# Kernel tuning notes

Measured on AMD Instinct MI355X. Metric: run time of the kernel, lower is better.

The kernel has to match this reference:

```python
import jax, jax.numpy as jnp
import numpy as np

# norse LIFParameters defaults
DT = 1e-3
TAU_SYN_INV = 200.0   # 1/5e-3
TAU_MEM_INV = 100.0   # 1/1e-2
V_TH = 1.0            # v_leak = v_reset = 0
ALPHA = 100.0         # SuperSpike surrogate slope
SEQ_LEN = 10
F_MAX = 1000.0

@jax.custom_vjp
def superspike(x):
    # forward: heaviside(x > 0); backward: SuperSpike surrogate
    return (x > 0).astype(x.dtype)

def _ss_fwd(x):
    return (x > 0).astype(x.dtype), x

def _ss_bwd(x, g):
    return (g / (ALPHA * jnp.abs(x) + 1.0) ** 2,)

superspike.defvjp(_ss_fwd, _ss_bwd)

def lif_step(x, z, v, i, w_in, w_rec):
    # norse lif_step: decay, threshold, reset, then integrate synaptic current
    v_dec = v + DT * TAU_MEM_INV * (-v + i)      # v_leak = 0
    i_dec = i - DT * TAU_SYN_INV * i
    z_new = superspike(v_dec - V_TH)
    v_new = (1.0 - z_new) * v_dec                # v_reset = 0
    i_new = i_dec + x @ w_in.T + z @ w_rec.T     # uses OLD z for recurrence
    return z_new, v_new, i_new

def setup_inputs() -> dict:
    key = jax.random.key(0)
    k1, k2, k3, k4, k5 = jax.random.split(key, 5)
    B = 1048576
    return {
        "input_tensor": jax.random.uniform(k1, (B, 12), dtype=jnp.float32),
        "w_in0": jax.random.normal(k2, (6, 12), jnp.float32) * np.float32(np.sqrt(2.0 / 12)),
        "w_rec0": jax.random.normal(k3, (6, 6), jnp.float32) * np.float32(np.sqrt(2.0 / 6)),
        "w_in1": jax.random.normal(k4, (1, 6), jnp.float32) * np.float32(np.sqrt(2.0 / 6)),
        "w_rec1": jax.random.normal(k5, (1, 1), jnp.float32) * np.float32(np.sqrt(2.0)),
    }

def reference(input_tensor, w_in0, w_rec0, w_in1, w_rec1):
    B = input_tensor.shape[0]
    dtype = input_tensor.dtype
    # PoissonEncoder: spike = (rand < dt * f_max * x), shape [T, B, 12]
    u = jax.random.uniform(jax.random.key(42), (SEQ_LEN,) + input_tensor.shape, dtype=dtype)
    spike_ts = (u < DT * F_MAX * input_tensor).astype(dtype)

    def step(carry, x_t):
        z0, v0, i0, z1, v1, i1 = carry
        z0n, v0n, i0n = lif_step(x_t, z0, v0, i0, w_in0, w_rec0)
        z1n, v1n, i1n = lif_step(z0n, z1, v1, i1, w_in1, w_rec1)
        return (z0n, v0n, i0n, z1n, v1n, i1n), None

    zeros = lambda n: jnp.zeros((B, n), dtype)
    init = (zeros(6), zeros(6), zeros(6), zeros(1), zeros(1), zeros(1))
    (z0, v0, i0, z1, v1, i1), _ = jax.lax.scan(step, init, spike_ts)
    return z1  # final-timestep output spikes, [B, 1]
```

## Files before the change

### kernel.cpp

```cpp
#include <hip/hip_runtime.h>
#include <cstdint>


#define TFR(r) { x0 += x1; x1 = __builtin_amdgcn_alignbit(x1, x1, 32 - (r)); x1 ^= x0; }

__device__ __forceinline__ uint32_t tf_hash(uint32_t c) {
  uint32_t x0 = 0u;
  uint32_t x1 = c + 42u;
  TFR(13) TFR(15) TFR(26) TFR(6)
  x0 += 42u;          x1 += 0x1BD11BF1u;
  TFR(17) TFR(29) TFR(16) TFR(24)
  x0 += 0x1BD11BF0u;  x1 += 2u;
  TFR(13) TFR(15) TFR(26) TFR(6)
         x1 += 45u;
  TFR(17) TFR(29) TFR(16) TFR(24)
  x0 += 42u;          x1 += 0x1BD11BF4u;
  TFR(13) TFR(15) TFR(26) TFR(6)
  x0 += 0x1BD11BF0u;  x1 += 5u;
  return x0 ^ x1;
}

__global__ __launch_bounds__(256) void build_tables(
    const float* __restrict__ w_in0, const float* __restrict__ w_rec0,
    const float* __restrict__ w_in1, float* __restrict__ ws)
{
  int m = blockIdx.x * 256 + threadIdx.x;
  float* tin = ws;
  float* trc = ws + 32768;
  float* tw1 = ws + 33280;
  #pragma unroll
  for (int n = 0; n < 6; ++n) {
    float acc = 0.0f;
    #pragma unroll
    for (int j = 0; j < 12; ++j)
      acc = __fmaf_rn(((m >> j) & 1) ? 1.0f : 0.0f, w_in0[n * 12 + j], acc);
    tin[(m << 3) + n] = acc;
  }
  if (m < 64) {
    #pragma unroll
    for (int n = 0; n < 6; ++n) {
      float acc = 0.0f;
      #pragma unroll
      for (int j = 0; j < 6; ++j)
        acc = __fmaf_rn(((m >> j) & 1) ? 1.0f : 0.0f, w_rec0[n * 6 + j], acc);
      trc[(m << 3) + n] = acc;
    }
    float acc = 0.0f;
    #pragma unroll
    for (int j = 0; j < 6; ++j)
      acc = __fmaf_rn(((m >> j) & 1) ? 1.0f : 0.0f, w_in1[j], acc);
    tw1[m] = acc;
  }
}

__global__ __launch_bounds__(256) void snn_kernel_tbl(
    const float* __restrict__ x_in, const float* __restrict__ w_rec1,
    const float* __restrict__ tbl, float* __restrict__ out, int B)
{
  int b = blockIdx.x * blockDim.x + threadIdx.x;
  if (b >= B) return;

  const float* __restrict__ tin = tbl;
  const float* __restrict__ trc = tbl + 32768;
  const float* __restrict__ tw1 = tbl + 33280;

  uint32_t TS[12];
  {
    const float4* xv = reinterpret_cast<const float4*>(x_in + (size_t)b * 12);
    float4 q0 = xv[0], q1 = xv[1], q2 = xv[2];
    float x[12] = {q0.x,q0.y,q0.z,q0.w, q1.x,q1.y,q1.z,q1.w, q2.x,q2.y,q2.z,q2.w};
    #pragma unroll
    for (int j = 0; j < 12; ++j)
      TS[j] = ((uint32_t)__builtin_ceilf(x[j] * 8388608.0f)) << 9;
  }

  const uint32_t t_stride = (uint32_t)B * 12u;
  uint32_t base = (uint32_t)b * 12u;
  uint32_t msk[8];
  #pragma unroll
  for (int t = 0; t < 8; ++t) {
    uint32_t m = 0;
    #pragma unroll
    for (int j = 0; j < 12; ++j) {
      uint32_t h = tf_hash(base + (uint32_t)j);
      m |= (h < TS[j]) ? (1u << j) : 0u;
    }
    msk[t] = m;
    base += t_stride;
  }

  float4 dA[8]; float2 dB[8];
  #pragma unroll
  for (int t = 0; t < 8; ++t) {
    const float* e = tin + (msk[t] << 3);
    dA[t] = *reinterpret_cast<const float4*>(e);
    dB[t] = *reinterpret_cast<const float2*>(e + 4);
  }

  float v0[6], i0[6];
  #pragma unroll
  for (int n = 0; n < 6; ++n) { v0[n] = 0.0f; i0[n] = 0.0f; }
  uint32_t zm = 0;
  float v1 = 0.0f, i1 = 0.0f, z1 = 0.0f;
  const float R1 = w_rec1[0];

  #pragma unroll
  for (int t = 0; t < 10; ++t) {
    uint32_t zmn = 0;
    if (t < 9) {
      float vdec[6];
      #pragma unroll
      for (int n = 0; n < 6; ++n) {
        vdec[n] = __fadd_rn(v0[n], __fmul_rn(0.1f, __fsub_rn(i0[n], v0[n])));
        zmn |= (vdec[n] > 1.0f) ? (1u << n) : 0u;
      }
      if (t < 8) {
        const float* rc = trc + (zm << 3);
        float4 r4 = *reinterpret_cast<const float4*>(rc);
        float2 r2 = *reinterpret_cast<const float2*>(rc + 4);
        float dR[6]  = {r4.x, r4.y, r4.z, r4.w, r2.x, r2.y};
        float dAv[6] = {dA[t].x, dA[t].y, dA[t].z, dA[t].w, dB[t].x, dB[t].y};
        #pragma unroll
        for (int n = 0; n < 6; ++n) {
          float idec = __fsub_rn(i0[n], __fmul_rn(0.2f, i0[n]));
          v0[n] = (vdec[n] > 1.0f) ? 0.0f : vdec[n];
          i0[n] = __fadd_rn(__fadd_rn(idec, dAv[n]), dR[n]);
        }
      }
    }
    {
      float vdec = __fadd_rn(v1, __fmul_rn(0.1f, __fsub_rn(i1, v1)));
      bool fire = (vdec > 1.0f);
      float z1n = fire ? 1.0f : 0.0f;
      if (t < 9) {
        float idec = __fsub_rn(i1, __fmul_rn(0.2f, i1));
        float d1 = tw1[zmn];
        float d2 = __fmaf_rn(z1, R1, 0.0f);
        i1 = __fadd_rn(__fadd_rn(idec, d1), d2);
        v1 = fire ? 0.0f : vdec;
      }
      z1 = z1n;
    }
    zm = zmn;
  }

  out[b] = z1;
}

__global__ __launch_bounds__(256) void snn_kernel(
    const float* __restrict__ x_in, const float* __restrict__ w_in0,
    const float* __restrict__ w_rec0, const float* __restrict__ w_in1,
    const float* __restrict__ w_rec1, float* __restrict__ out, int B)
{
  int b = blockIdx.x * blockDim.x + threadIdx.x;
  if (b >= B) return;

  uint32_t T[12];
  {
    const float4* xv = reinterpret_cast<const float4*>(x_in + (size_t)b * 12);
    float4 q0 = xv[0], q1 = xv[1], q2 = xv[2];
    float x[12] = {q0.x,q0.y,q0.z,q0.w, q1.x,q1.y,q1.z,q1.w, q2.x,q2.y,q2.z,q2.w};
    #pragma unroll
    for (int j = 0; j < 12; ++j)
      T[j] = (uint32_t)__builtin_ceilf(x[j] * 8388608.0f);
  }

  float W0[6][12], R0[6][6], W1[6], R1;
  #pragma unroll
  for (int n = 0; n < 6; ++n) {
    #pragma unroll
    for (int j = 0; j < 12; ++j) W0[n][j] = w_in0[n * 12 + j];
  }
  #pragma unroll
  for (int n = 0; n < 6; ++n) {
    #pragma unroll
    for (int j = 0; j < 6; ++j) R0[n][j] = w_rec0[n * 6 + j];
  }
  #pragma unroll
  for (int j = 0; j < 6; ++j) W1[j] = w_in1[j];
  R1 = w_rec1[0];

  float v0[6], i0[6], z0[6];
  #pragma unroll
  for (int n = 0; n < 6; ++n) { v0[n] = 0.0f; i0[n] = 0.0f; z0[n] = 0.0f; }
  float v1 = 0.0f, i1 = 0.0f, z1 = 0.0f;

  const uint32_t t_stride = (uint32_t)B * 12u;
  uint32_t base = (uint32_t)b * 12u;

  #pragma unroll
  for (int t = 0; t < 10; ++t) {
    float sp[12];
    #pragma unroll
    for (int j = 0; j < 12; ++j) {
      uint32_t h = tf_hash(base + (uint32_t)j);
      sp[j] = ((h >> 9) < T[j]) ? 1.0f : 0.0f;
    }
    base += t_stride;

    float zn[6], vn[6], inew[6];
    #pragma unroll
    for (int n = 0; n < 6; ++n) {
      float vdec = __fadd_rn(v0[n], __fmul_rn(0.1f, __fsub_rn(i0[n], v0[n])));
      float idec = __fsub_rn(i0[n], __fmul_rn(0.2f, i0[n]));
      bool fire = (vdec > 1.0f);
      zn[n] = fire ? 1.0f : 0.0f;
      vn[n] = fire ? 0.0f : vdec;
      float d1 = 0.0f;
      #pragma unroll
      for (int j = 0; j < 12; ++j) d1 = __fmaf_rn(sp[j], W0[n][j], d1);
      float d2 = 0.0f;
      #pragma unroll
      for (int j = 0; j < 6; ++j) d2 = __fmaf_rn(z0[j], R0[n][j], d2);
      inew[n] = __fadd_rn(__fadd_rn(idec, d1), d2);
    }
    {
      float vdec = __fadd_rn(v1, __fmul_rn(0.1f, __fsub_rn(i1, v1)));
      float idec = __fsub_rn(i1, __fmul_rn(0.2f, i1));
      bool fire = (vdec > 1.0f);
      float z1n = fire ? 1.0f : 0.0f;
      float v1n = fire ? 0.0f : vdec;
      float d1 = 0.0f;
      #pragma unroll
      for (int j = 0; j < 6; ++j) d1 = __fmaf_rn(zn[j], W1[j], d1);
      float d2 = __fmaf_rn(z1, R1, 0.0f);
      float i1n = __fadd_rn(__fadd_rn(idec, d1), d2);
      z1 = z1n; v1 = v1n; i1 = i1n;
    }
    #pragma unroll
    for (int n = 0; n < 6; ++n) { z0[n] = zn[n]; v0[n] = vn[n]; i0[n] = inew[n]; }
  }

  out[b] = z1;
}

extern "C" void kernel_launch(void* const* d_in, const int* in_sizes, int n_in,
                              void* d_out, int out_size, void* d_ws, size_t ws_size,
                              hipStream_t stream) {
  const float* x      = (const float*)d_in[0];
  const float* w_in0  = (const float*)d_in[1];
  const float* w_rec0 = (const float*)d_in[2];
  const float* w_in1  = (const float*)d_in[3];
  const float* w_rec1 = (const float*)d_in[4];
  float* out = (float*)d_out;

  const int B = out_size;
  const int block = 256;
  const int grid = (B + block - 1) / block;

  const size_t WS_NEEDED = (size_t)(33280 + 64) * sizeof(float);
  if (d_ws != nullptr && ws_size >= WS_NEEDED) {
    float* tbl = (float*)d_ws;
    build_tables<<<16, 256, 0, stream>>>(w_in0, w_rec0, w_in1, tbl);
    snn_kernel_tbl<<<grid, block, 0, stream>>>(x, w_rec1, tbl, out, B);
  } else {
    snn_kernel<<<grid, block, 0, stream>>>(x, w_in0, w_rec0, w_in1, w_rec1, out, B);
  }
}
```

Before: 266.7 us.

## Interleave Poisson mask hashing with LIF recurrence and use inline-asm bit accumulation

Instead of computing all eight timestep spike masks and table gathers up front, the kernel now computes masks two steps ahead and interleaves the hash work with the recurrent LIF updates. The recurrent-table gather is issued right after each step's spike mask is known, and the first and last timesteps are peeled. Inline GCN asm (v_cmp plus v_addc) accumulates mask and fire bits with fewer instructions. The goal is to cut register pressure and hide gather latency behind ALU-heavy hashing. The cost is hand-written asm that clobbers vcc and reversed bit order that has to stay consistent with the table layout.

Measured after the change: 259.8 us. 2.6% less time.

```diff
diff --git a/kernel.cpp b/kernel.cpp
--- a/kernel.cpp
+++ b/kernel.cpp
@@ -20,6 +20,38 @@
   return x0 ^ x1;
 }
 
+__device__ __forceinline__ void mask_acc(uint32_t& m, uint32_t h, uint32_t ts) {
+  asm("v_cmp_lt_u32 vcc, %1, %2\n\t"
+      "v_addc_co_u32 %0, vcc, %0, %0, vcc"
+      : "+v"(m) : "v"(h), "v"(ts) : "vcc");
+}
+
+__device__ __forceinline__ void fire_acc(uint32_t& zm, float& vout, float vdec, float fzero) {
+  asm("v_cmp_lt_f32 vcc, 1.0, %2\n\t"
+      "v_cndmask_b32 %1, %2, %3, vcc\n\t"
+      "v_addc_co_u32 %0, vcc, %0, %0, vcc"
+      : "+v"(zm), "=&v"(vout) : "v"(vdec), "v"(fzero) : "vcc");
+}
+
+__device__ __forceinline__ void fire_bit(uint32_t& zm, float vdec) {
+  asm("v_cmp_lt_f32 vcc, 1.0, %1\n\t"
+      "v_addc_co_u32 %0, vcc, %0, %0, vcc"
+      : "+v"(zm) : "v"(vdec) : "vcc");
+}
+
+__device__ __forceinline__ uint32_t mask12(uint32_t cbase, const uint32_t (&TS)[12]) {
+  uint32_t m = 0;
+  #pragma unroll
+  for (int j = 11; j >= 0; --j)
+    mask_acc(m, tf_hash(cbase + (uint32_t)j), TS[j]);
+  return m;
+}
+
+__device__ __forceinline__ void gather6(const float* __restrict__ row, float4& a, float2& b) {
+  a = *reinterpret_cast<const float4*>(row);
+  b = *reinterpret_cast<const float2*>(row + 4);
+}
+
 __global__ __launch_bounds__(256) void build_tables(
     const float* __restrict__ w_in0, const float* __restrict__ w_rec0,
     const float* __restrict__ w_in1, float* __restrict__ ws)
@@ -75,73 +107,91 @@
   }
 
   const uint32_t t_stride = (uint32_t)B * 12u;
-  uint32_t base = (uint32_t)b * 12u;
-  uint32_t msk[8];
-  #pragma unroll
-  for (int t = 0; t < 8; ++t) {
-    uint32_t m = 0;
-    #pragma unroll
-    for (int j = 0; j < 12; ++j) {
-      uint32_t h = tf_hash(base + (uint32_t)j);
-      m |= (h < TS[j]) ? (1u << j) : 0u;
-    }
-    msk[t] = m;
-    base += t_stride;
-  }
-
-  float4 dA[8]; float2 dB[8];
-  #pragma unroll
-  for (int t = 0; t < 8; ++t) {
-    const float* e = tin + (msk[t] << 3);
-    dA[t] = *reinterpret_cast<const float4*>(e);
-    dB[t] = *reinterpret_cast<const float2*>(e + 4);
-  }
-
-  float v0[6], i0[6];
-  #pragma unroll
-  for (int n = 0; n < 6; ++n) { v0[n] = 0.0f; i0[n] = 0.0f; }
-  uint32_t zm = 0;
+  const uint32_t c0 = (uint32_t)b * 12u;
+  float fzero = 0.0f;
+
+  float4 A[8]; float2 Bv[8];
+
+  uint32_t msk0 = mask12(c0, TS);
+  uint32_t msk1 = mask12(c0 + t_stride, TS);
+  gather6(tin + (msk0 << 3), A[0], Bv[0]);
+  gather6(tin + (msk1 << 3), A[1], Bv[1]);
+
+  float v0[6] = {0,0,0,0,0,0};
+  float i0[6] = {A[0].x, A[0].y, A[0].z, A[0].w, Bv[0].x, Bv[0].y};
   float v1 = 0.0f, i1 = 0.0f, z1 = 0.0f;
   const float R1 = w_rec1[0];
 
-  #pragma unroll
-  for (int t = 0; t < 10; ++t) {
+  {
+    uint32_t mk = mask12(c0 + 2u * t_stride, TS);
+    gather6(tin + (mk << 3), A[2], Bv[2]);
+  }
+
+  float dR[6] = {0,0,0,0,0,0};
+
+  #pragma unroll
+  for (int t = 1; t <= 7; ++t) {
+    float vd[6], vnew[6];
     uint32_t zmn = 0;
-    if (t < 9) {
-      float vdec[6];
-      #pragma unroll
-      for (int n = 0; n < 6; ++n) {
-        vdec[n] = __fadd_rn(v0[n], __fmul_rn(0.1f, __fsub_rn(i0[n], v0[n])));
-        zmn |= (vdec[n] > 1.0f) ? (1u << n) : 0u;
-      }
-      if (t < 8) {
-        const float* rc = trc + (zm << 3);
-        float4 r4 = *reinterpret_cast<const float4*>(rc);
-        float2 r2 = *reinterpret_cast<const float2*>(rc + 4);
-        float dR[6]  = {r4.x, r4.y, r4.z, r4.w, r2.x, r2.y};
-        float dAv[6] = {dA[t].x, dA[t].y, dA[t].z, dA[t].w, dB[t].x, dB[t].y};
-        #pragma unroll
-        for (int n = 0; n < 6; ++n) {
-          float idec = __fsub_rn(i0[n], __fmul_rn(0.2f, i0[n]));
-          v0[n] = (vdec[n] > 1.0f) ? 0.0f : vdec[n];
-          i0[n] = __fadd_rn(__fadd_rn(idec, dAv[n]), dR[n]);
-        }
-      }
-    }
+    #pragma unroll
+    for (int n = 0; n < 6; ++n)
+      vd[n] = __fadd_rn(v0[n], __fmul_rn(0.1f, __fsub_rn(i0[n], v0[n])));
+    #pragma unroll
+    for (int n = 5; n >= 0; --n)
+      fire_acc(zmn, vnew[n], vd[n], fzero);
+
+    float w1g = tw1[zmn];
+    float4 r4; float2 r2;
+    if (t <= 6) gather6(trc + (zmn << 3), r4, r2);
+
+    float dAv[6] = {A[t].x, A[t].y, A[t].z, A[t].w, Bv[t].x, Bv[t].y};
+    #pragma unroll
+    for (int n = 0; n < 6; ++n) {
+      float idec = __fsub_rn(i0[n], __fmul_rn(0.2f, i0[n]));
+      float s = __fadd_rn(idec, dAv[n]);
+      i0[n] = (t == 1) ? s : __fadd_rn(s, dR[n]);
+      v0[n] = vnew[n];
+    }
+
+    if (t <= 5) {
+      uint32_t mk = mask12(c0 + (uint32_t)(t + 2) * t_stride, TS);
+      gather6(tin + (mk << 3), A[t + 2], Bv[t + 2]);
+    }
+
     {
       float vdec = __fadd_rn(v1, __fmul_rn(0.1f, __fsub_rn(i1, v1)));
-      bool fire = (vdec > 1.0f);
+      bool fire = vdec > 1.0f;
       float z1n = fire ? 1.0f : 0.0f;
-      if (t < 9) {
-        float idec = __fsub_rn(i1, __fmul_rn(0.2f, i1));
-        float d1 = tw1[zmn];
-        float d2 = __fmaf_rn(z1, R1, 0.0f);
-        i1 = __fadd_rn(__fadd_rn(idec, d1), d2);
-        v1 = fire ? 0.0f : vdec;
-      }
+      float idec = __fsub_rn(i1, __fmul_rn(0.2f, i1));
+      float d2 = __fmaf_rn(z1, R1, 0.0f);
+      i1 = __fadd_rn(__fadd_rn(idec, w1g), d2);
+      v1 = fire ? 0.0f : vdec;
       z1 = z1n;
     }
-    zm = zmn;
+
+    dR[0]=r4.x; dR[1]=r4.y; dR[2]=r4.z; dR[3]=r4.w; dR[4]=r2.x; dR[5]=r2.y;
+  }
+
+  {
+    uint32_t zmn = 0;
+    #pragma unroll
+    for (int n = 5; n >= 0; --n) {
+      float vd = __fadd_rn(v0[n], __fmul_rn(0.1f, __fsub_rn(i0[n], v0[n])));
+      fire_bit(zmn, vd);
+    }
+    float w1g = tw1[zmn];
+    float vdec = __fadd_rn(v1, __fmul_rn(0.1f, __fsub_rn(i1, v1)));
+    bool fire = vdec > 1.0f;
+    float z1n = fire ? 1.0f : 0.0f;
+    float idec = __fsub_rn(i1, __fmul_rn(0.2f, i1));
+    float d2 = __fmaf_rn(z1, R1, 0.0f);
+    i1 = __fadd_rn(__fadd_rn(idec, w1g), d2);
+    v1 = fire ? 0.0f : vdec;
+    z1 = z1n;
+  }
+  {
+    float vdec = __fadd_rn(v1, __fmul_rn(0.1f, __fsub_rn(i1, v1)));
+    z1 = (vdec > 1.0f) ? 1.0f : 0.0f;
   }
 
   out[b] = z1;
```
